# Performance work log

Hardware: AMD Instinct MI355X
Metric: run time of the kernel (lower is better)

## Reference

```python
import jax, jax.numpy as jnp
import numpy as np

N = 4_000_000   # number of sparse voxels
H = 128         # parent-grid extent per axis (input coords < 256 -> parents < 128)


def setup_inputs() -> dict:
    key = jax.random.key(0)
    # col 0 = batch index, cols 1:4 = integer xyz voxel coords in [0, 256)
    coords = jax.random.randint(key, (N, 4), 0, 256, dtype=jnp.int32)
    # spnn.Conv3d(1,1,k=2) kernel: (2^3, in=1, out=1), constant-init to 1.0
    kernel = jnp.ones((8, 1, 1), dtype=jnp.float32)
    return {"coords": coords, "kernel": kernel}


def _fog(coords, kernel):
    b = coords[:, 0].astype(jnp.int64)
    xyz = coords[:, 1:]
    # pos(): 3-bit occupancy code from LSBs of xyz, feat = 2^code
    bits = xyz & 1                                        # (N, 3)
    pos = bits[:, 0] + 2 * bits[:, 1] + 4 * bits[:, 2]    # (N,) in [0, 8)
    feats = (jnp.int32(1) << pos).astype(jnp.float32)     # (N,) values {1,...,128}

    # 2x2x2 stride-2 sparse conv with all-ones kernel == sum over the 8 children
    # of each parent voxel. The child's kernel-offset index is exactly `pos`.
    pxyz = (xyz >> 1).astype(jnp.int64)                   # parent coords
    pkey = ((b * H + pxyz[:, 0]) * H + pxyz[:, 1]) * H + pxyz[:, 2]

    ukeys, inv = jnp.unique(pkey, size=N, fill_value=-1, return_inverse=True)
    inv = inv.ravel()

    contrib = feats * kernel[pos, 0, 0]                   # all-ones kernel -> feats
    out_feats = jax.ops.segment_sum(contrib, inv, num_segments=N)  # (N,)

    # decode unique parent keys back to (batch, x, y, z); pad slots -> -1
    valid = ukeys >= 0
    k = jnp.where(valid, ukeys, 0)
    oz = k % H
    k = k // H
    oy = k % H
    k = k // H
    ox = k % H
    ob = k // H
    out_coords = jnp.stack([ob, ox, oy, oz], axis=-1).astype(jnp.int32)
    out_coords = jnp.where(valid[:, None], out_coords, jnp.int32(-1))
    return out_coords, out_feats


def reference(coords, kernel):
    return _fog(coords, kernel)
```

## Files before the change

### kernel.cpp

```cpp
#include <hip/hip_runtime.h>

#define NB_BITS     14
#define N_BUCKETS   (1 << NB_BITS)
#define LOCAL_BITS  15
#define LOCAL_WORDS (1 << (LOCAL_BITS - 5))
#define LKMASK      ((1u << LOCAL_BITS) - 1u)
#define KEYMASK     0x1FFFFFFFu
#define NBLK        256
#define N_PART      8
#define STASH       512
#define BPB         8
#define EGRID       (N_BUCKETS / BPB)

__device__ __forceinline__ unsigned make_key(int4 c) {
    return ((((unsigned)c.x << 7) | (unsigned)(c.y >> 1)) << 7 | (unsigned)(c.z >> 1)) << 7
         | (unsigned)(c.w >> 1);
}

template<int NW>
__device__ inline void block_scan(unsigned v, unsigned* wsum, unsigned& excl, unsigned& total) {
    int t = threadIdx.x, ln = t & 63, wv = t >> 6;
    unsigned incl = v;
    #pragma unroll
    for (int off = 1; off < 64; off <<= 1) {
        unsigned y = __shfl_up(incl, off, 64);
        if (ln >= off) incl += y;
    }
    if (ln == 63) wsum[wv] = incl;
    __syncthreads();
    if (wv == 0) {
        unsigned s = (ln < NW) ? wsum[ln] : 0u;
        #pragma unroll
        for (int off = 1; off < NW; off <<= 1) {
            unsigned y = __shfl_up(s, off, 64);
            if (ln >= off) s += y;
        }
        if (ln < NW) wsum[ln] = s;
    }
    __syncthreads();
    excl = (wv ? wsum[wv - 1] : 0u) + incl - v;
    total = wsum[NW - 1];
}

__global__ void hist_pass(const int4* __restrict__ coords,
                          unsigned* __restrict__ hist,
                          unsigned* __restrict__ skeys, int n, int chunk) {
    __shared__ unsigned h[N_BUCKETS];
    int k = blockIdx.x, t = threadIdx.x;
    for (int i = t; i < N_BUCKETS; i += 1024) h[i] = 0u;
    __syncthreads();
    int s = k * chunk, e = min(n, s + chunk);
    for (int i = s + t; i < e; i += 1024) {
        int4 c = coords[i];
        unsigned key = make_key(c);
        unsigned pos = (unsigned)((c.y & 1) | ((c.z & 1) << 1) | ((c.w & 1) << 2));
        skeys[i] = (pos << 29) | key;
        atomicAdd(&h[key >> LOCAL_BITS], 1u);
    }
    __syncthreads();
    for (int i = t; i < N_BUCKETS; i += 1024) hist[k * N_BUCKETS + i] = h[i];
}

__global__ void offs_pass(const unsigned* __restrict__ hist,
                          unsigned* __restrict__ offs,
                          unsigned* __restrict__ total) {
    int b = blockIdx.x * blockDim.x + threadIdx.x;
    unsigned run = 0;
    #pragma unroll 1
    for (int g = 0; g < N_PART; ++g)
        for (int j = 0; j < NBLK / N_PART; ++j) {
            int k = j * N_PART + g;
            offs[k * N_BUCKETS + b] = run;
            run += hist[k * N_BUCKETS + b];
        }
    total[b] = run;
}

__global__ void scan16k(const unsigned* __restrict__ in, unsigned* __restrict__ out) {
    __shared__ unsigned wsum[16];
    int t = threadIdx.x;
    unsigned v[16], sum = 0;
    #pragma unroll
    for (int i = 0; i < 16; ++i) { v[i] = in[t * 16 + i]; sum += v[i]; }
    unsigned excl, tot;
    block_scan<16>(sum, wsum, excl, tot);
    unsigned run = excl;
    #pragma unroll
    for (int i = 0; i < 16; ++i) { out[t * 16 + i] = run; run += v[i]; }
    if (t == 1023) out[N_BUCKETS] = run;
}

__global__ void scatter_pass(const unsigned* __restrict__ skeys,
                             const unsigned* __restrict__ offs,
                             const unsigned* __restrict__ pbase,
                             unsigned* __restrict__ pairs, int n, int chunk) {
    __shared__ unsigned cur[N_BUCKETS];
    int k = blockIdx.x, t = threadIdx.x;
    for (int i = t; i < N_BUCKETS; i += 1024)
        cur[i] = pbase[i] + offs[k * N_BUCKETS + i];
    __syncthreads();
    int s = k * chunk, e = min(n, s + chunk);
    for (int i = s + t; i < e; i += 1024) {
        unsigned pk = skeys[i];
        unsigned b = (pk & KEYMASK) >> LOCAL_BITS;
        unsigned j = atomicAdd(&cur[b], 1u);
        pairs[j] = pk;
    }
}

__global__ void __launch_bounds__(256, 8)
count8(const unsigned* __restrict__ pairs,
       const unsigned* __restrict__ pbase,
       unsigned* __restrict__ ucount) {
    __shared__ unsigned bm[LOCAL_WORDS];
    __shared__ unsigned wsum[4];
    __shared__ unsigned sb[BPB + 1];
    int t = threadIdx.x, g = blockIdx.x;
    if (t < BPB + 1) sb[t] = pbase[g * BPB + t];
    ((uint4*)bm)[t] = make_uint4(0u, 0u, 0u, 0u);
    __syncthreads();
    #pragma unroll 1
    for (int j = 0; j < BPB; ++j) {
        unsigned s = sb[j], e = sb[j + 1];
        for (unsigned i = s + t; i < e; i += 256) {
            unsigned k = pairs[i] & LKMASK;
            atomicOr(&bm[k >> 5], 1u << (k & 31u));
        }
        __syncthreads();
        uint4 w = ((uint4*)bm)[t];
        ((uint4*)bm)[t] = make_uint4(0u, 0u, 0u, 0u);
        unsigned v = __popc(w.x) + __popc(w.y) + __popc(w.z) + __popc(w.w);
        int ln = t & 63, wv = t >> 6;
        #pragma unroll
        for (int off = 1; off < 64; off <<= 1) v += __shfl_xor(v, off, 64);
        if (ln == 0) wsum[wv] = v;
        __syncthreads();
        if (t == 0) ucount[g * BPB + j] = wsum[0] + wsum[1] + wsum[2] + wsum[3];
    }
}

__global__ void __launch_bounds__(256, 8)
emit8(const unsigned* __restrict__ pairs,
      const unsigned* __restrict__ pbase,
      const unsigned* __restrict__ ubase,
      const float* __restrict__ kern,
      float4* __restrict__ out_coords,
      float* __restrict__ out_feats, int n) {
    __shared__ unsigned bm[LOCAL_WORDS];
    __shared__ unsigned pfx[LOCAL_WORDS];
    __shared__ float    fe[STASH];
    __shared__ unsigned skl[STASH];
    __shared__ unsigned wsum[4];
    __shared__ unsigned sb[BPB + 1], ub[BPB];
    __shared__ float    kl[8];
    int t = threadIdx.x, g = blockIdx.x;
    if (t < BPB + 1) sb[t] = pbase[g * BPB + t];
    if (t < BPB) ub[t] = ubase[g * BPB + t];
    if (t < 8) kl[t] = (float)(1 << t) * kern[t];
    ((uint4*)bm)[t] = make_uint4(0u, 0u, 0u, 0u);
    fe[t] = 0.f; fe[t + 256] = 0.f;
    __syncthreads();
    #pragma unroll 1
    for (int j = 0; j < BPB; ++j) {
        unsigned s = sb[j], e = sb[j + 1];
        for (unsigned i = s + t; i < e; i += 256) {
            unsigned pk = pairs[i];
            unsigned li = i - s;
            if (li < STASH) skl[li] = pk;
            unsigned k = pk & LKMASK;
            atomicOr(&bm[k >> 5], 1u << (k & 31u));
        }
        __syncthreads();
        uint4 w = ((uint4*)bm)[t];
        unsigned pc0 = __popc(w.x), pc1 = __popc(w.y), pc2 = __popc(w.z), pc3 = __popc(w.w);
        unsigned excl, count;
        block_scan<4>(pc0 + pc1 + pc2 + pc3, wsum, excl, count);
        unsigned run = excl;
        uint4 p;
        p.x = run; run += pc0; p.y = run; run += pc1; p.z = run; run += pc2; p.w = run;
        ((uint4*)pfx)[t] = p;
        __syncthreads();
        unsigned npts = e - s;
        for (unsigned li = t; li < npts; li += 256) {
            unsigned pk = skl[li];
            unsigned k = pk & LKMASK;
            unsigned lr = pfx[k >> 5] + __popc(bm[k >> 5] & ((1u << (k & 31u)) - 1u));
            atomicAdd(&fe[lr], kl[pk >> 29]);
        }
        __syncthreads();
        unsigned base = ub[j];
        unsigned ws[4] = { w.x, w.y, w.z, w.w };
        unsigned rs[4] = { p.x, p.y, p.z, p.w };
        unsigned bbits = ((unsigned)g * BPB + (unsigned)j) << LOCAL_BITS;
        #pragma unroll
        for (int q = 0; q < 4; ++q) {
            unsigned bits = ws[q], r = rs[q];
            unsigned wi = 4u * t + q;
            while (bits) {
                int bit = __ffs(bits) - 1;
                bits &= bits - 1;
                unsigned key = bbits | (wi << 5) | (unsigned)bit;
                out_coords[base + r] = make_float4((float)(key >> 21),
                                                   (float)((key >> 14) & 127u),
                                                   (float)((key >> 7) & 127u),
                                                   (float)(key & 127u));
                ++r;
            }
        }
        for (unsigned i = t; i < count; i += 256) {
            out_feats[base + i] = fe[i];
            fe[i] = 0.f;
        }
        ((uint4*)bm)[t] = make_uint4(0u, 0u, 0u, 0u);
        __syncthreads();
    }
    unsigned total = ubase[N_BUCKETS];
    for (unsigned r = total + (unsigned)(g * 256 + t); r < (unsigned)n; r += EGRID * 256u) {
        out_coords[r] = make_float4(-1.f, -1.f, -1.f, -1.f);
        out_feats[r] = 0.f;
    }
}

extern "C" void kernel_launch(void* const* d_in, const int* in_sizes, int n_in,
                              void* d_out, int out_size, void* d_ws, size_t ws_size,
                              hipStream_t stream) {
    const int4* coords = (const int4*)d_in[0];
    const float* kern  = (const float*)d_in[1];
    int N = in_sizes[0] / 4;

    float* out = (float*)d_out;
    float4* out_coords = (float4*)out;
    float* out_feats = out + (size_t)4 * N;

    unsigned* pairs = (unsigned*)d_ws;
    unsigned* skeys = pairs + (size_t)N;
    unsigned* hist  = skeys + (size_t)N;
    unsigned* offs  = hist + (size_t)NBLK * N_BUCKETS;
    unsigned* total = offs + (size_t)NBLK * N_BUCKETS;
    unsigned* pbase = total + N_BUCKETS;
    unsigned* ucount = pbase + (N_BUCKETS + 1);
    unsigned* ubase  = ucount + N_BUCKETS;

    int chunk = (N + NBLK - 1) / NBLK;
    hist_pass<<<NBLK, 1024, 0, stream>>>(coords, hist, skeys, N, chunk);
    offs_pass<<<N_BUCKETS / 256, 256, 0, stream>>>(hist, offs, total);
    scan16k<<<1, 1024, 0, stream>>>(total, pbase);
    scatter_pass<<<NBLK, 1024, 0, stream>>>(skeys, offs, pbase, pairs, N, chunk);
    count8<<<EGRID, 256, 0, stream>>>(pairs, pbase, ucount);
    scan16k<<<1, 1024, 0, stream>>>(ucount, ubase);
    emit8<<<EGRID, 256, 0, stream>>>(pairs, pbase, ubase, kern, out_coords, out_feats, N);
}
```

Measured before the change: 238.6 us.

## Process one bucket per wavefront in count and emit kernels

```diff
diff --git a/kernel.cpp b/kernel.cpp
--- a/kernel.cpp
+++ b/kernel.cpp
@@ -8,9 +8,9 @@
 #define KEYMASK     0x1FFFFFFFu
 #define NBLK        256
 #define N_PART      8
-#define STASH       512
-#define BPB         8
-#define EGRID       (N_BUCKETS / BPB)
+#define FE_CAP      384
+#define WPB         4
+#define EGRID       (N_BUCKETS / WPB)
 
 __device__ __forceinline__ unsigned make_key(int4 c) {
     return ((((unsigned)c.x << 7) | (unsigned)(c.y >> 1)) << 7 | (unsigned)(c.z >> 1)) << 7
@@ -109,113 +109,106 @@
 }
 
 __global__ void __launch_bounds__(256, 8)
-count8(const unsigned* __restrict__ pairs,
+count_w(const unsigned* __restrict__ pairs,
+        const unsigned* __restrict__ pbase,
+        unsigned* __restrict__ ucount) {
+    __shared__ unsigned bm[WPB][LOCAL_WORDS];
+    int t = threadIdx.x, ln = t & 63, wv = t >> 6;
+    int b = blockIdx.x * WPB + wv;
+    uint4* bm4 = (uint4*)bm[wv];
+    uint4 z = make_uint4(0u, 0u, 0u, 0u);
+    #pragma unroll
+    for (int m = 0; m < 4; ++m) bm4[ln * 4 + m] = z;
+    unsigned s = pbase[b], e = pbase[b + 1];
+    for (unsigned i = s + ln; i < e; i += 64) {
+        unsigned k = pairs[i] & LKMASK;
+        atomicOr(&bm[wv][k >> 5], 1u << (k & 31u));
+    }
+    unsigned v = 0;
+    #pragma unroll
+    for (int m = 0; m < 4; ++m) {
+        uint4 q = bm4[ln * 4 + m];
+        v += __popc(q.x) + __popc(q.y) + __popc(q.z) + __popc(q.w);
+    }
+    #pragma unroll
+    for (int off = 1; off < 64; off <<= 1) v += __shfl_xor(v, off, 64);
+    if (ln == 0) ucount[b] = v;
+}
+
+__global__ void __launch_bounds__(256, 4)
+emit_w(const unsigned* __restrict__ pairs,
        const unsigned* __restrict__ pbase,
-       unsigned* __restrict__ ucount) {
-    __shared__ unsigned bm[LOCAL_WORDS];
-    __shared__ unsigned wsum[4];
-    __shared__ unsigned sb[BPB + 1];
-    int t = threadIdx.x, g = blockIdx.x;
-    if (t < BPB + 1) sb[t] = pbase[g * BPB + t];
-    ((uint4*)bm)[t] = make_uint4(0u, 0u, 0u, 0u);
-    __syncthreads();
-    #pragma unroll 1
-    for (int j = 0; j < BPB; ++j) {
-        unsigned s = sb[j], e = sb[j + 1];
-        for (unsigned i = s + t; i < e; i += 256) {
-            unsigned k = pairs[i] & LKMASK;
-            atomicOr(&bm[k >> 5], 1u << (k & 31u));
+       const unsigned* __restrict__ ubase,
+       const float* __restrict__ kern,
+       float4* __restrict__ out_coords,
+       float* __restrict__ out_feats, int n) {
+    __shared__ unsigned bm[WPB][LOCAL_WORDS];
+    __shared__ unsigned pfx[WPB][LOCAL_WORDS];
+    __shared__ float    fe[WPB][FE_CAP];
+    int t = threadIdx.x, ln = t & 63, wv = t >> 6;
+    int b = blockIdx.x * WPB + wv;
+    uint4* bm4 = (uint4*)bm[wv];
+    uint4* pfx4 = (uint4*)pfx[wv];
+    uint4 z = make_uint4(0u, 0u, 0u, 0u);
+    #pragma unroll
+    for (int m = 0; m < 4; ++m) bm4[ln * 4 + m] = z;
+    for (int i = ln; i < FE_CAP; i += 64) fe[wv][i] = 0.f;
+    unsigned s = pbase[b], e = pbase[b + 1];
+    for (unsigned i = s + ln; i < e; i += 64) {
+        unsigned k = pairs[i] & LKMASK;
+        atomicOr(&bm[wv][k >> 5], 1u << (k & 31u));
+    }
+    unsigned w[16];
+    #pragma unroll
+    for (int m = 0; m < 4; ++m) {
+        uint4 q = bm4[ln * 4 + m];
+        w[4 * m] = q.x; w[4 * m + 1] = q.y; w[4 * m + 2] = q.z; w[4 * m + 3] = q.w;
+    }
+    unsigned ssum = 0;
+    #pragma unroll
+    for (int m = 0; m < 16; ++m) ssum += __popc(w[m]);
+    unsigned incl = ssum;
+    #pragma unroll
+    for (int off = 1; off < 64; off <<= 1) {
+        unsigned y = __shfl_up(incl, off, 64);
+        if (ln >= off) incl += y;
+    }
+    unsigned count = __shfl(incl, 63, 64);
+    unsigned run = incl - ssum;
+    unsigned pv[16];
+    #pragma unroll
+    for (int m = 0; m < 16; ++m) { pv[m] = run; run += __popc(w[m]); }
+    #pragma unroll
+    for (int m = 0; m < 4; ++m)
+        pfx4[ln * 4 + m] = make_uint4(pv[4 * m], pv[4 * m + 1], pv[4 * m + 2], pv[4 * m + 3]);
+    for (unsigned i = s + ln; i < e; i += 64) {
+        unsigned pk = pairs[i];
+        unsigned k = pk & LKMASK;
+        unsigned pos = pk >> 29;
+        unsigned lr = pfx[wv][k >> 5] + __popc(bm[wv][k >> 5] & ((1u << (k & 31u)) - 1u));
+        atomicAdd(&fe[wv][lr], (float)(1 << pos) * kern[pos]);
+    }
+    unsigned base = ubase[b];
+    unsigned bbits = (unsigned)b << LOCAL_BITS;
+    #pragma unroll
+    for (int m = 0; m < 16; ++m) {
+        unsigned bits = w[m], r = pv[m];
+        unsigned wi = (unsigned)(ln * 16 + m);
+        while (bits) {
+            int bit = __ffs(bits) - 1;
+            bits &= bits - 1;
+            unsigned key = bbits | (wi << 5) | (unsigned)bit;
+            out_coords[base + r] = make_float4((float)(key >> 21),
+                                               (float)((key >> 14) & 127u),
+                                               (float)((key >> 7) & 127u),
+                                               (float)(key & 127u));
+            ++r;
         }
-        __syncthreads();
-        uint4 w = ((uint4*)bm)[t];
-        ((uint4*)bm)[t] = make_uint4(0u, 0u, 0u, 0u);
-        unsigned v = __popc(w.x) + __popc(w.y) + __popc(w.z) + __popc(w.w);
-        int ln = t & 63, wv = t >> 6;
-        #pragma unroll
-        for (int off = 1; off < 64; off <<= 1) v += __shfl_xor(v, off, 64);
-        if (ln == 0) wsum[wv] = v;
-        __syncthreads();
-        if (t == 0) ucount[g * BPB + j] = wsum[0] + wsum[1] + wsum[2] + wsum[3];
-    }
-}
-
-__global__ void __launch_bounds__(256, 8)
-emit8(const unsigned* __restrict__ pairs,
-      const unsigned* __restrict__ pbase,
-      const unsigned* __restrict__ ubase,
-      const float* __restrict__ kern,
-      float4* __restrict__ out_coords,
-      float* __restrict__ out_feats, int n) {
-    __shared__ unsigned bm[LOCAL_WORDS];
-    __shared__ unsigned pfx[LOCAL_WORDS];
-    __shared__ float    fe[STASH];
-    __shared__ unsigned skl[STASH];
-    __shared__ unsigned wsum[4];
-    __shared__ unsigned sb[BPB + 1], ub[BPB];
-    __shared__ float    kl[8];
-    int t = threadIdx.x, g = blockIdx.x;
-    if (t < BPB + 1) sb[t] = pbase[g * BPB + t];
-    if (t < BPB) ub[t] = ubase[g * BPB + t];
-    if (t < 8) kl[t] = (float)(1 << t) * kern[t];
-    ((uint4*)bm)[t] = make_uint4(0u, 0u, 0u, 0u);
-    fe[t] = 0.f; fe[t + 256] = 0.f;
-    __syncthreads();
-    #pragma unroll 1
-    for (int j = 0; j < BPB; ++j) {
-        unsigned s = sb[j], e = sb[j + 1];
-        for (unsigned i = s + t; i < e; i += 256) {
-            unsigned pk = pairs[i];
-            unsigned li = i - s;
-            if (li < STASH) skl[li] = pk;
-            unsigned k = pk & LKMASK;
-            atomicOr(&bm[k >> 5], 1u << (k & 31u));
-        }
-        __syncthreads();
-        uint4 w = ((uint4*)bm)[t];
-        unsigned pc0 = __popc(w.x), pc1 = __popc(w.y), pc2 = __popc(w.z), pc3 = __popc(w.w);
-        unsigned excl, count;
-        block_scan<4>(pc0 + pc1 + pc2 + pc3, wsum, excl, count);
-        unsigned run = excl;
-        uint4 p;
-        p.x = run; run += pc0; p.y = run; run += pc1; p.z = run; run += pc2; p.w = run;
-        ((uint4*)pfx)[t] = p;
-        __syncthreads();
-        unsigned npts = e - s;
-        for (unsigned li = t; li < npts; li += 256) {
-            unsigned pk = skl[li];
-            unsigned k = pk & LKMASK;
-            unsigned lr = pfx[k >> 5] + __popc(bm[k >> 5] & ((1u << (k & 31u)) - 1u));
-            atomicAdd(&fe[lr], kl[pk >> 29]);
-        }
-        __syncthreads();
-        unsigned base = ub[j];
-        unsigned ws[4] = { w.x, w.y, w.z, w.w };
-        unsigned rs[4] = { p.x, p.y, p.z, p.w };
-        unsigned bbits = ((unsigned)g * BPB + (unsigned)j) << LOCAL_BITS;
-        #pragma unroll
-        for (int q = 0; q < 4; ++q) {
-            unsigned bits = ws[q], r = rs[q];
-            unsigned wi = 4u * t + q;
-            while (bits) {
-                int bit = __ffs(bits) - 1;
-                bits &= bits - 1;
-                unsigned key = bbits | (wi << 5) | (unsigned)bit;
-                out_coords[base + r] = make_float4((float)(key >> 21),
-                                                   (float)((key >> 14) & 127u),
-                                                   (float)((key >> 7) & 127u),
-                                                   (float)(key & 127u));
-                ++r;
-            }
-        }
-        for (unsigned i = t; i < count; i += 256) {
-            out_feats[base + i] = fe[i];
-            fe[i] = 0.f;
-        }
-        ((uint4*)bm)[t] = make_uint4(0u, 0u, 0u, 0u);
-        __syncthreads();
-    }
+    }
+    for (unsigned i = ln; i < count; i += 64)
+        out_feats[base + i] = fe[wv][i];
     unsigned total = ubase[N_BUCKETS];
-    for (unsigned r = total + (unsigned)(g * 256 + t); r < (unsigned)n; r += EGRID * 256u) {
+    for (unsigned r = total + (unsigned)(blockIdx.x * 256 + t); r < (unsigned)n; r += EGRID * 256u) {
         out_coords[r] = make_float4(-1.f, -1.f, -1.f, -1.f);
         out_feats[r] = 0.f;
     }
@@ -246,7 +239,7 @@
     offs_pass<<<N_BUCKETS / 256, 256, 0, stream>>>(hist, offs, total);
     scan16k<<<1, 1024, 0, stream>>>(total, pbase);
     scatter_pass<<<NBLK, 1024, 0, stream>>>(skeys, offs, pbase, pairs, N, chunk);
-    count8<<<EGRID, 256, 0, stream>>>(pairs, pbase, ucount);
+    count_w<<<EGRID, 256, 0, stream>>>(pairs, pbase, ucount);
     scan16k<<<1, 1024, 0, stream>>>(ucount, ubase);
-    emit8<<<EGRID, 256, 0, stream>>>(pairs, pbase, ubase, kern, out_coords, out_feats, N);
-}
+    emit_w<<<EGRID, 256, 0, stream>>>(pairs, pbase, ubase, kern, out_coords, out_feats, N);
+}
```

Measured after the change: 238.7 us. Within noise of the previous version (+0.1%).

## Pack 16-bit histograms, fuse scans into scatter/emit, emit coords per point

Applied to the files above, without the earlier changes.

```diff
diff --git a/kernel.cpp b/kernel.cpp
--- a/kernel.cpp
+++ b/kernel.cpp
@@ -3,7 +3,7 @@
 #define NB_BITS     14
 #define N_BUCKETS   (1 << NB_BITS)
 #define LOCAL_BITS  15
-#define LOCAL_WORDS (1 << (LOCAL_BITS - 5))
+#define LOCAL_WORDS 1024
 #define LKMASK      ((1u << LOCAL_BITS) - 1u)
 #define KEYMASK     0x1FFFFFFFu
 #define NBLK        256
@@ -43,11 +43,11 @@
 }
 
 __global__ void hist_pass(const int4* __restrict__ coords,
-                          unsigned* __restrict__ hist,
+                          unsigned* __restrict__ hist32,
                           unsigned* __restrict__ skeys, int n, int chunk) {
-    __shared__ unsigned h[N_BUCKETS];
+    __shared__ unsigned h[8192];
     int k = blockIdx.x, t = threadIdx.x;
-    for (int i = t; i < N_BUCKETS; i += 1024) h[i] = 0u;
+    for (int i = t; i < 8192; i += 1024) h[i] = 0u;
     __syncthreads();
     int s = k * chunk, e = min(n, s + chunk);
     for (int i = s + t; i < e; i += 1024) {
@@ -55,55 +55,61 @@
         unsigned key = make_key(c);
         unsigned pos = (unsigned)((c.y & 1) | ((c.z & 1) << 1) | ((c.w & 1) << 2));
         skeys[i] = (pos << 29) | key;
-        atomicAdd(&h[key >> LOCAL_BITS], 1u);
-    }
-    __syncthreads();
-    for (int i = t; i < N_BUCKETS; i += 1024) hist[k * N_BUCKETS + i] = h[i];
-}
-
-__global__ void offs_pass(const unsigned* __restrict__ hist,
-                          unsigned* __restrict__ offs,
+        unsigned b = key >> LOCAL_BITS;
+        atomicAdd(&h[b >> 1], (b & 1) ? 65536u : 1u);
+    }
+    __syncthreads();
+    for (int i = t; i < 8192; i += 1024) hist32[k * 8192 + i] = h[i];
+}
+
+__global__ void offs_pass(const unsigned* __restrict__ hist32,
+                          unsigned* __restrict__ offs32,
                           unsigned* __restrict__ total) {
-    int b = blockIdx.x * blockDim.x + threadIdx.x;
-    unsigned run = 0;
+    int gid = blockIdx.x * blockDim.x + threadIdx.x;
+    unsigned r0 = 0, r1 = 0;
     #pragma unroll 1
     for (int g = 0; g < N_PART; ++g)
         for (int j = 0; j < NBLK / N_PART; ++j) {
-            int k = j * N_PART + g;
-            offs[k * N_BUCKETS + b] = run;
-            run += hist[k * N_BUCKETS + b];
-        }
-    total[b] = run;
-}
-
-__global__ void scan16k(const unsigned* __restrict__ in, unsigned* __restrict__ out) {
+            int kk = j * N_PART + g;
+            unsigned h = hist32[kk * 8192 + gid];
+            offs32[kk * 8192 + gid] = r0 | (r1 << 16);
+            r0 += h & 0xFFFFu; r1 += h >> 16;
+        }
+    total[2 * gid] = r0;
+    total[2 * gid + 1] = r1;
+}
+
+__global__ void __launch_bounds__(1024)
+scatter_pass(const unsigned* __restrict__ skeys,
+             const unsigned* __restrict__ offs32,
+             const unsigned* __restrict__ total,
+             unsigned* __restrict__ pbase,
+             unsigned* __restrict__ pairs, int n, int chunk) {
+    __shared__ unsigned buf[N_BUCKETS];
     __shared__ unsigned wsum[16];
-    int t = threadIdx.x;
+    int t = threadIdx.x, k = blockIdx.x;
     unsigned v[16], sum = 0;
     #pragma unroll
-    for (int i = 0; i < 16; ++i) { v[i] = in[t * 16 + i]; sum += v[i]; }
+    for (int i = 0; i < 16; ++i) { v[i] = total[t * 16 + i]; sum += v[i]; }
     unsigned excl, tot;
     block_scan<16>(sum, wsum, excl, tot);
     unsigned run = excl;
     #pragma unroll
-    for (int i = 0; i < 16; ++i) { out[t * 16 + i] = run; run += v[i]; }
-    if (t == 1023) out[N_BUCKETS] = run;
-}
-
-__global__ void scatter_pass(const unsigned* __restrict__ skeys,
-                             const unsigned* __restrict__ offs,
-                             const unsigned* __restrict__ pbase,
-                             unsigned* __restrict__ pairs, int n, int chunk) {
-    __shared__ unsigned cur[N_BUCKETS];
-    int k = blockIdx.x, t = threadIdx.x;
+    for (int i = 0; i < 16; ++i) {
+        buf[t * 16 + i] = run;
+        if (k == 0) pbase[t * 16 + i] = run;
+        run += v[i];
+    }
+    if (k == 0 && t == 1023) pbase[N_BUCKETS] = run;
+    __syncthreads();
     for (int i = t; i < N_BUCKETS; i += 1024)
-        cur[i] = pbase[i] + offs[k * N_BUCKETS + i];
+        buf[i] += (offs32[k * 8192 + (i >> 1)] >> ((i & 1) * 16)) & 0xFFFFu;
     __syncthreads();
     int s = k * chunk, e = min(n, s + chunk);
     for (int i = s + t; i < e; i += 1024) {
         unsigned pk = skeys[i];
         unsigned b = (pk & KEYMASK) >> LOCAL_BITS;
-        unsigned j = atomicAdd(&cur[b], 1u);
+        unsigned j = atomicAdd(&buf[b], 1u);
         pairs[j] = pk;
     }
 }
@@ -140,22 +146,46 @@
 }
 
 __global__ void __launch_bounds__(256, 8)
-emit8(const unsigned* __restrict__ pairs,
-      const unsigned* __restrict__ pbase,
-      const unsigned* __restrict__ ubase,
-      const float* __restrict__ kern,
-      float4* __restrict__ out_coords,
-      float* __restrict__ out_feats, int n) {
+emit_f(const unsigned* __restrict__ pairs,
+       const unsigned* __restrict__ pbase,
+       const unsigned* __restrict__ ucount,
+       const float* __restrict__ kern,
+       float4* __restrict__ out_coords,
+       float* __restrict__ out_feats, int n) {
     __shared__ unsigned bm[LOCAL_WORDS];
     __shared__ unsigned pfx[LOCAL_WORDS];
     __shared__ float    fe[STASH];
     __shared__ unsigned skl[STASH];
     __shared__ unsigned wsum[4];
-    __shared__ unsigned sb[BPB + 1], ub[BPB];
+    __shared__ unsigned sb[BPB + 1];
+    __shared__ unsigned ubS[BPB];
     __shared__ float    kl[8];
     int t = threadIdx.x, g = blockIdx.x;
+    const uint4* uc4 = (const uint4*)ucount;
+    unsigned usum = 0;
+    #pragma unroll
+    for (int m = 0; m < 16; ++m) {
+        uint4 q = uc4[t * 16 + m];
+        usum += q.x + q.y + q.z + q.w;
+    }
+    unsigned uexcl, totalU;
+    block_scan<4>(usum, wsum, uexcl, totalU);
+    if (t == (g >> 3)) {
+        int o = (g & 7) * 8;
+        unsigned r = uexcl;
+        #pragma unroll 1
+        for (int m = 0; m < 16; ++m) {
+            uint4 q = uc4[t * 16 + m];
+            unsigned a[4] = { q.x, q.y, q.z, q.w };
+            #pragma unroll
+            for (int jj = 0; jj < 4; ++jj) {
+                int j = 4 * m + jj;
+                if (j >= o && j < o + 8) ubS[j - o] = r;
+                r += a[jj];
+            }
+        }
+    }
     if (t < BPB + 1) sb[t] = pbase[g * BPB + t];
-    if (t < BPB) ub[t] = ubase[g * BPB + t];
     if (t < 8) kl[t] = (float)(1 << t) * kern[t];
     ((uint4*)bm)[t] = make_uint4(0u, 0u, 0u, 0u);
     fe[t] = 0.f; fe[t + 256] = 0.f;
@@ -181,32 +211,20 @@
         ((uint4*)pfx)[t] = p;
         __syncthreads();
         unsigned npts = e - s;
+        unsigned base = ubS[j];
         for (unsigned li = t; li < npts; li += 256) {
-            unsigned pk = skl[li];
-            unsigned k = pk & LKMASK;
-            unsigned lr = pfx[k >> 5] + __popc(bm[k >> 5] & ((1u << (k & 31u)) - 1u));
+            unsigned pk = (li < STASH) ? skl[li] : pairs[s + li];
+            unsigned key = pk & KEYMASK;
+            unsigned lk = key & LKMASK;
+            unsigned wd = lk >> 5;
+            unsigned lr = pfx[wd] + __popc(bm[wd] & ((1u << (lk & 31u)) - 1u));
             atomicAdd(&fe[lr], kl[pk >> 29]);
-        }
-        __syncthreads();
-        unsigned base = ub[j];
-        unsigned ws[4] = { w.x, w.y, w.z, w.w };
-        unsigned rs[4] = { p.x, p.y, p.z, p.w };
-        unsigned bbits = ((unsigned)g * BPB + (unsigned)j) << LOCAL_BITS;
-        #pragma unroll
-        for (int q = 0; q < 4; ++q) {
-            unsigned bits = ws[q], r = rs[q];
-            unsigned wi = 4u * t + q;
-            while (bits) {
-                int bit = __ffs(bits) - 1;
-                bits &= bits - 1;
-                unsigned key = bbits | (wi << 5) | (unsigned)bit;
-                out_coords[base + r] = make_float4((float)(key >> 21),
-                                                   (float)((key >> 14) & 127u),
-                                                   (float)((key >> 7) & 127u),
-                                                   (float)(key & 127u));
-                ++r;
-            }
-        }
+            out_coords[base + lr] = make_float4((float)(key >> 21),
+                                                (float)((key >> 14) & 127u),
+                                                (float)((key >> 7) & 127u),
+                                                (float)(key & 127u));
+        }
+        __syncthreads();
         for (unsigned i = t; i < count; i += 256) {
             out_feats[base + i] = fe[i];
             fe[i] = 0.f;
@@ -214,8 +232,7 @@
         ((uint4*)bm)[t] = make_uint4(0u, 0u, 0u, 0u);
         __syncthreads();
     }
-    unsigned total = ubase[N_BUCKETS];
-    for (unsigned r = total + (unsigned)(g * 256 + t); r < (unsigned)n; r += EGRID * 256u) {
+    for (unsigned r = totalU + (unsigned)(g * 256 + t); r < (unsigned)n; r += EGRID * 256u) {
         out_coords[r] = make_float4(-1.f, -1.f, -1.f, -1.f);
         out_feats[r] = 0.f;
     }
@@ -232,21 +249,18 @@
     float4* out_coords = (float4*)out;
     float* out_feats = out + (size_t)4 * N;
 
-    unsigned* pairs = (unsigned*)d_ws;
-    unsigned* skeys = pairs + (size_t)N;
-    unsigned* hist  = skeys + (size_t)N;
-    unsigned* offs  = hist + (size_t)NBLK * N_BUCKETS;
-    unsigned* total = offs + (size_t)NBLK * N_BUCKETS;
-    unsigned* pbase = total + N_BUCKETS;
-    unsigned* ucount = pbase + (N_BUCKETS + 1);
-    unsigned* ubase  = ucount + N_BUCKETS;
+    unsigned* pairs  = (unsigned*)d_ws;
+    unsigned* skeys  = pairs + (size_t)N;
+    unsigned* hist32 = skeys + (size_t)N;
+    unsigned* offs32 = hist32 + (size_t)NBLK * 8192;
+    unsigned* total  = offs32 + (size_t)NBLK * 8192;
+    unsigned* pbase  = total + N_BUCKETS;
+    unsigned* ucount = pbase + 16400;
 
     int chunk = (N + NBLK - 1) / NBLK;
-    hist_pass<<<NBLK, 1024, 0, stream>>>(coords, hist, skeys, N, chunk);
-    offs_pass<<<N_BUCKETS / 256, 256, 0, stream>>>(hist, offs, total);
-    scan16k<<<1, 1024, 0, stream>>>(total, pbase);
-    scatter_pass<<<NBLK, 1024, 0, stream>>>(skeys, offs, pbase, pairs, N, chunk);
+    hist_pass<<<NBLK, 1024, 0, stream>>>(coords, hist32, skeys, N, chunk);
+    offs_pass<<<32, 256, 0, stream>>>(hist32, offs32, total);
+    scatter_pass<<<NBLK, 1024, 0, stream>>>(skeys, offs32, total, pbase, pairs, N, chunk);
     count8<<<EGRID, 256, 0, stream>>>(pairs, pbase, ucount);
-    scan16k<<<1, 1024, 0, stream>>>(ucount, ubase);
-    emit8<<<EGRID, 256, 0, stream>>>(pairs, pbase, ubase, kern, out_coords, out_feats, N);
-}
+    emit_f<<<EGRID, 256, 0, stream>>>(pairs, pbase, ucount, kern, out_coords, out_feats, N);
+}
```

After: 243.5 us. 1.02x slower.
